# Kernel optimization log

Measured on AMD Instinct MI355X. Metric: run time of the kernel, lower is better.

Reference implementation:

```python
import jax, jax.numpy as jnp
import numpy as np

B, C, H, W = 32, 64, 64, 64
K = 512  # n_embeddings
D = 64   # embedding_dim


def setup_inputs() -> dict:
    key = jax.random.key(0)
    k1, k2 = jax.random.split(key)
    inputs = jax.random.normal(k1, (B, C, H, W), dtype=jnp.float32)
    embedding = jax.random.normal(k2, (K, D), dtype=jnp.float32)
    weight = jnp.ones((K,), dtype=jnp.float32)
    return {"inputs": inputs, "embedding": embedding, "weight": weight}


def reference(inputs, embedding, weight):
    # NCHW -> NHWC, flatten to [N, D]
    x = jnp.transpose(inputs, (0, 2, 3, 1))  # [B,H,W,D]
    input_shape = x.shape
    flat = x.reshape(-1, D)                  # [N,D], N = B*H*W
    n = flat.shape[0]

    usage = jnp.sum(weight >= 0.01)

    # squared Euclidean distances (argmin-equivalent to torch.cdist)
    d2 = (jnp.sum(flat * flat, axis=1, keepdims=True)
          - 2.0 * (flat @ embedding.T)
          + jnp.sum(embedding * embedding, axis=1))  # [N,K]
    indices = jnp.argmin(d2, axis=1)                 # [N]

    # one-hot assignment stats (scatter -> bincount form)
    counts = jnp.zeros((K,), dtype=flat.dtype).at[indices].add(1.0)
    avg_probs = counts / n
    perplexity = jnp.exp(-jnp.sum(avg_probs * jnp.log(avg_probs + 1e-10)))

    # straight-through quantization
    q = embedding[indices].reshape(input_shape)      # [B,H,W,D]
    quantized = jax.lax.stop_gradient(q) + x - jax.lax.stop_gradient(x)

    commitment_loss = jnp.mean((jax.lax.stop_gradient(quantized) - x) ** 2)

    quantized_nchw = jnp.transpose(quantized, (0, 3, 1, 2))
    return quantized_nchw, commitment_loss, perplexity, usage, indices
```

## Files before the change

kernel.cpp:

```cpp
#include <hip/hip_runtime.h>


typedef __attribute__((ext_vector_type(8))) _Float16 f16x8;
typedef __attribute__((ext_vector_type(4))) float f32x4;
typedef unsigned int uint;
typedef unsigned short ushort;

namespace {
constexpr int kC = 64, kH = 64, kW = 64;
constexpr int kK = 512, kD = 64;
constexpr int kHW = kH * kW;
constexpr int kCHW = kC * kHW;
constexpr int kN = 32 * kHW;
constexpr int kQElems = 32 * kC * kHW;
constexpr uint kGapFP = 21u;
}

__device__ __forceinline__ ushort hb(_Float16 h) { return __builtin_bit_cast(ushort, h); }
__device__ __forceinline__ uint umin(uint a, uint b) { return a < b ? a : b; }
__device__ __forceinline__ uint umax(uint a, uint b) { return a > b ? a : b; }

__device__ __forceinline__ void gld16(const void* g, void* l) {
  __builtin_amdgcn_global_load_lds(
      (const __attribute__((address_space(1))) uint*)g,
      (__attribute__((address_space(3))) uint*)l, 16, 0, 0);
}

__global__ __launch_bounds__(64) void vq_prep(const float* __restrict__ emb,
                                              ushort* __restrict__ embPh,
                                              ushort* __restrict__ embPl,
                                              float* __restrict__ enorm,
                                              uint* __restrict__ counts,
                                              uint* __restrict__ flag_count) {
  const int k = blockIdx.x * 64 + threadIdx.x;
  const float4* __restrict__ ep4 = (const float4*)(emb + k * kD);
  uint uh[32], ul[32];
  float s = 0.f;
#pragma unroll
  for (int j = 0; j < kD / 4; ++j) {
    const float4 v = ep4[j];
    s = fmaf(v.x, v.x, s); s = fmaf(v.y, v.y, s);
    s = fmaf(v.z, v.z, s); s = fmaf(v.w, v.w, s);
    const float e0 = v.x * 2048.f, e1 = v.y * 2048.f;
    const float e2 = v.z * 2048.f, e3 = v.w * 2048.f;
    const _Float16 h0 = (_Float16)e0, h1 = (_Float16)e1;
    const _Float16 h2 = (_Float16)e2, h3 = (_Float16)e3;
    const _Float16 l0 = (_Float16)(e0 - (float)h0);
    const _Float16 l1 = (_Float16)(e1 - (float)h1);
    const _Float16 l2 = (_Float16)(e2 - (float)h2);
    const _Float16 l3 = (_Float16)(e3 - (float)h3);
    uh[2 * j] = (uint)hb(h0) | ((uint)hb(h1) << 16);
    uh[2 * j + 1] = (uint)hb(h2) | ((uint)hb(h3) << 16);
    ul[2 * j] = (uint)hb(l0) | ((uint)hb(l1) << 16);
    ul[2 * j + 1] = (uint)hb(l2) | ((uint)hb(l3) << 16);
  }
  uint4* __restrict__ ph4 = (uint4*)embPh;
  uint4* __restrict__ pl4 = (uint4*)embPl;
#pragma unroll
  for (int cc = 0; cc < 8; ++cc) {
    const int dst = k * 8 + (cc ^ (k & 7));
    ph4[dst] = uint4{uh[4 * cc], uh[4 * cc + 1], uh[4 * cc + 2], uh[4 * cc + 3]};
    pl4[dst] = uint4{ul[4 * cc], ul[4 * cc + 1], ul[4 * cc + 2], ul[4 * cc + 3]};
  }
  enorm[k] = s;
  counts[k] = 0u;
  if (k == 0) *flag_count = 0u;
}

__global__ __launch_bounds__(512, 4) void vq_assign(
    const float* __restrict__ in, const float* __restrict__ emb,
    const ushort* __restrict__ embPh, const ushort* __restrict__ embPl,
    const float* __restrict__ enorm, float* __restrict__ idx_out,
    float* __restrict__ outq, uint* __restrict__ counts,
    float* __restrict__ partial, uint* __restrict__ flag_count,
    uint* __restrict__ flags, uint flag_cap) {
  __shared__ __align__(16) char lds[74240];
  char* __restrict__ xbh = lds;
  char* __restrict__ xbl = lds + 16384;
  char* __restrict__ ebh = lds + 32768;
  char* __restrict__ ebl = lds + 49152;
  uint* __restrict__ mm1 = (uint*)(lds + 65536);
  uint* __restrict__ mm2 = (uint*)(lds + 67584);
  float* __restrict__ xnp = (float*)(lds + 69632);
  uint* __restrict__ hist = (uint*)(lds + 71680);
  uint* __restrict__ fidx = (uint*)(lds + 73728);
  float* __restrict__ ldsE = (float*)lds;

  const int tid = threadIdx.x;
  const int lane = tid & 63;
  const int wv = __builtin_amdgcn_readfirstlane(tid >> 6);
  const int ph = wv >> 2;
  const int cs = wv & 3;
  const int c = lane & 15;
  const int g = lane >> 4;

  const int blk = blockIdx.x;
  const int bb = blk >> 5;
  const int hw0 = (blk & 31) << 7;
  const float* __restrict__ xp = in + (size_t)bb * kCHW + hw0 + ph * 64;

  hist[tid] = 0u;

  auto stageE = [&](int buf, int st) {
    const size_t src = (size_t)st * 8192 + cs * 2048;
    const int dst = buf * 8192 + cs * 2048;
#pragma unroll
    for (int i = 0; i < 2; ++i) {
      gld16((const char*)embPh + src + i * 1024 + lane * 16, ebh + dst + i * 1024);
      gld16((const char*)embPl + src + i * 1024 + lane * 16, ebl + dst + i * 1024);
    }
  };
  stageE(0, 0);

  float en_pre[8];
#pragma unroll
  for (int st = 0; st < 8; ++st)
    en_pre[st] = (enorm[st * 64 + cs * 16 + c] + 256.f) * 2048.f;

  {
    const int p = lane;
    uint uh[8], ul[8];
    float xn = 0.f;
#pragma unroll
    for (int j = 0; j < 8; ++j) {
      const float f0 = xp[(size_t)(cs * 16 + 2 * j) * kHW + p];
      const float f1 = xp[(size_t)(cs * 16 + 2 * j + 1) * kHW + p];
      xn = fmaf(f0, f0, xn);
      xn = fmaf(f1, f1, xn);
      const float m0 = -2.f * f0, m1f = -2.f * f1;
      const _Float16 h0 = (_Float16)m0, h1 = (_Float16)m1f;
      const _Float16 l0 = (_Float16)(m0 - (float)h0);
      const _Float16 l1 = (_Float16)(m1f - (float)h1);
      uh[j] = (uint)hb(h0) | ((uint)hb(h1) << 16);
      ul[j] = (uint)hb(l0) | ((uint)hb(l1) << 16);
    }
    const int row = ph * 64 + p;
    const int swz = (row & 7) << 4;
    const int o0 = (row * 128 + cs * 32) ^ swz;
    const int o1 = (row * 128 + cs * 32 + 16) ^ swz;
    *(uint4*)(xbh + o0) = uint4{uh[0], uh[1], uh[2], uh[3]};
    *(uint4*)(xbh + o1) = uint4{uh[4], uh[5], uh[6], uh[7]};
    *(uint4*)(xbl + o0) = uint4{ul[0], ul[1], ul[2], ul[3]};
    *(uint4*)(xbl + o1) = uint4{ul[4], ul[5], ul[6], ul[7]};
    xnp[cs * 128 + row] = xn;
  }
  __syncthreads();

  uint m1[16], m2[16];
#pragma unroll
  for (int i = 0; i < 16; ++i) { m1[i] = 0xFFFFFFFFu; m2[i] = 0xFFFFFFFFu; }

#pragma unroll
  for (int st = 0; st < 8; ++st) {
    if (st < 7) stageE((st & 1) ^ 1, st + 1);

    if (st < 7) {
      asm volatile("s_waitcnt vmcnt(4)" ::: "memory");
    } else {
      asm volatile("s_waitcnt vmcnt(0)" ::: "memory");
    }
    __builtin_amdgcn_sched_barrier(0);

    const int rowb = cs * 16 + c;
    const int swb = (rowb & 7) << 4;
    const int bbase = (st & 1) * 8192;
    const int ob0 = bbase + ((rowb * 128 + g * 16) ^ swb);
    const int ob1 = bbase + ((rowb * 128 + g * 16 + 64) ^ swb);
    const f16x8 bh0 = *(const f16x8*)(ebh + ob0);
    const f16x8 bh1 = *(const f16x8*)(ebh + ob1);
    const f16x8 bl0 = *(const f16x8*)(ebl + ob0);
    const f16x8 bl1 = *(const f16x8*)(ebl + ob1);
    const float en = en_pre[st];
    const uint kor = (uint)(st * 64 + cs * 16 + c);
    __builtin_amdgcn_s_setprio(1);
#pragma unroll
    for (int rt = 0; rt < 4; ++rt) {
      f16x8 ah[2], al[2];
#pragma unroll
      for (int s = 0; s < 2; ++s) {
        const int row = ph * 64 + rt * 16 + c;
        const int off = (row * 128 + g * 16 + s * 64) ^ ((row & 7) << 4);
        ah[s] = *(const f16x8*)(xbh + off);
        al[s] = *(const f16x8*)(xbl + off);
      }
      f32x4 acc0 = {en, en, en, en};
      f32x4 acc1 = {0.f, 0.f, 0.f, 0.f};
      acc0 = __builtin_amdgcn_mfma_f32_16x16x32_f16(ah[0], bh0, acc0, 0, 0, 0);
      acc1 = __builtin_amdgcn_mfma_f32_16x16x32_f16(ah[1], bh1, acc1, 0, 0, 0);
      acc0 = __builtin_amdgcn_mfma_f32_16x16x32_f16(ah[0], bl0, acc0, 0, 0, 0);
      acc1 = __builtin_amdgcn_mfma_f32_16x16x32_f16(ah[1], bl1, acc1, 0, 0, 0);
      acc0 = __builtin_amdgcn_mfma_f32_16x16x32_f16(al[0], bh0, acc0, 0, 0, 0);
      acc1 = __builtin_amdgcn_mfma_f32_16x16x32_f16(al[1], bh1, acc1, 0, 0, 0);
#pragma unroll
      for (int r = 0; r < 4; ++r) {
        const uint u = ((uint)(acc0[r] + acc1[r]) << 9) | kor;
        const int i = rt * 4 + r;
        const uint t = umax(m1[i], u);
        m1[i] = umin(m1[i], u);
        m2[i] = umin(m2[i], t);
      }
    }
    __builtin_amdgcn_s_setprio(0);

    asm volatile("s_waitcnt lgkmcnt(0)" ::: "memory");
    __builtin_amdgcn_sched_barrier(0);
    __builtin_amdgcn_s_barrier();
  }

#pragma unroll
  for (int i = 0; i < 16; ++i) {
    uint a1 = m1[i], a2 = m2[i];
#pragma unroll
    for (int off = 1; off < 16; off <<= 1) {
      const uint o1 = __shfl_xor(a1, off, 64);
      const uint o2 = __shfl_xor(a2, off, 64);
      const uint t = umax(a1, o1);
      a1 = umin(a1, o1);
      a2 = umin(umin(a2, o2), t);
    }
    m1[i] = a1; m2[i] = a2;
  }

  if (c == 0) {
#pragma unroll
    for (int i = 0; i < 16; ++i) {
      const int p = ph * 64 + (i >> 2) * 16 + g * 4 + (i & 3);
      mm1[cs * 128 + p] = m1[i];
      mm2[cs * 128 + p] = m2[i];
    }
  }
  __syncthreads();

  if (tid < 128) {
    uint a1 = mm1[tid], a2 = mm2[tid];
#pragma unroll
    for (int s = 1; s < 4; ++s) {
      const uint u1 = mm1[s * 128 + tid], u2 = mm2[s * 128 + tid];
      const uint t = umax(a1, u1);
      a1 = umin(a1, u1);
      a2 = umin(umin(a2, u2), t);
    }
    const uint bidx = a1 & 511u;
    fidx[tid] = bidx;
    idx_out[blk * 128 + tid] = (float)bidx;
    if (((a2 >> 9) - (a1 >> 9)) < kGapFP) {
      const uint slot = atomicAdd(flag_count, 1u);
      if (slot < flag_cap) flags[slot] = (uint)(blk * 128 + tid);
    }
    atomicAdd(&hist[bidx], 1u);

    const float xnorm = (xnp[tid] + xnp[128 + tid]) + (xnp[256 + tid] + xnp[384 + tid]);
    float d2 = fmaf((float)(a1 >> 9), 1.f / 2048.f, -256.f) + xnorm;
#pragma unroll
    for (int off = 32; off > 0; off >>= 1) d2 += __shfl_down(d2, off, 64);
    if ((tid & 63) == 0) partial[blk * 2 + (tid >> 6)] = d2;
  }
  __syncthreads();
  if (hist[tid]) atomicAdd(&counts[tid], hist[tid]);

#pragma unroll
  for (int pass = 0; pass < 4; ++pass) {
    const int r = pass * 32 + (tid >> 4);
    const int q = tid & 15;
    const float4 v = *(const float4*)(emb + fidx[r] * kD + q * 4);
    const int cswz = (q * 4) ^ (((r >> 4) & 7) << 3);
    *(float4*)(ldsE + r * 64 + cswz) = v;
  }
  __syncthreads();
  {
    const int ch = tid >> 3;
    const int wq = tid & 7;
    float* __restrict__ oq = outq + (size_t)bb * kCHW + (size_t)ch * kHW + hw0 + wq * 16;
    float4 vv[4];
#pragma unroll
    for (int i = 0; i < 16; ++i) {
      const int p = wq * 16 + i;
      const int cswz = ch ^ (((p >> 4) & 7) << 3);
      ((float*)vv)[i] = ldsE[p * 64 + cswz];
    }
#pragma unroll
    for (int i = 0; i < 4; ++i) *(float4*)(oq + i * 4) = vv[i];
  }
}

__global__ __launch_bounds__(256) void vq_refine_fin(
    const float* __restrict__ in, const float* __restrict__ emb,
    const float* __restrict__ weight, const uint* __restrict__ flag_count,
    const uint* __restrict__ flags, uint flag_cap, float* __restrict__ idx_out,
    float* __restrict__ outq, const uint* __restrict__ counts,
    const float* __restrict__ partial, float* __restrict__ out_scalars) {
  if (blockIdx.x == 256) {
    __shared__ float red[256];
    const int t = threadIdx.x;

    {
      const float a0 = (float)counts[t] / (float)kN;
      const float a1 = (float)counts[t + 256] / (float)kN;
      red[t] = a0 * logf(a0 + 1e-10f) + a1 * logf(a1 + 1e-10f);
    }
    __syncthreads();
#pragma unroll
    for (int off = 128; off > 0; off >>= 1) {
      if (t < off) red[t] += red[t + off];
      __syncthreads();
    }
    const float perp = expf(-red[0]);
    __syncthreads();

    {
      float a = 0.f;
#pragma unroll
      for (int j = 0; j < 8; ++j) a += partial[t + 256 * j];
      red[t] = a;
    }
    __syncthreads();
#pragma unroll
    for (int off = 128; off > 0; off >>= 1) {
      if (t < off) red[t] += red[t + off];
      __syncthreads();
    }
    const float loss = red[0] / (float)((long long)kN * (long long)kD);
    __syncthreads();

    red[t] = ((weight[t] >= 0.01f) ? 1.f : 0.f) +
             ((weight[t + 256] >= 0.01f) ? 1.f : 0.f);
    __syncthreads();
#pragma unroll
    for (int off = 128; off > 0; off >>= 1) {
      if (t < off) red[t] += red[t + off];
      __syncthreads();
    }
    if (t == 0) {
      out_scalars[0] = loss;
      out_scalars[1] = perp;
      out_scalars[2] = red[0];
    }
    return;
  }

  uint cnt = *flag_count;
  if (cnt > flag_cap) cnt = flag_cap;
  const int lane = threadIdx.x & 63;
  const uint wave_id = blockIdx.x * 4u + (threadIdx.x >> 6);
  const uint wave_stride = 256u * 4u;

  for (uint i = wave_id; i < cnt; i += wave_stride) {
    const int n = (int)flags[i];
    const int b = n >> 12;
    const int hw = n & 4095;
    const float* __restrict__ xp = in + (size_t)b * kCHW + hw;

    float xr[kD];
#pragma unroll
    for (int d = 0; d < kD; ++d) xr[d] = xp[(size_t)d * kHW];

    double best = 1e300;
    int bidx = 0;
#pragma unroll 1
    for (int kk = 0; kk < 8; ++kk) {
      const int k = lane * 8 + kk;
      const float4* __restrict__ ep4 = (const float4*)(emb + k * kD);
      double s0 = 0.0, s1 = 0.0;
#pragma unroll
      for (int j = 0; j < kD / 4; ++j) {
        const float4 e = ep4[j];
        const double d0 = (double)xr[4 * j + 0] - (double)e.x;
        const double d1 = (double)xr[4 * j + 1] - (double)e.y;
        const double d2 = (double)xr[4 * j + 2] - (double)e.z;
        const double d3 = (double)xr[4 * j + 3] - (double)e.w;
        s0 = fma(d0, d0, s0);
        s1 = fma(d1, d1, s1);
        s0 = fma(d2, d2, s0);
        s1 = fma(d3, d3, s1);
      }
      const double s = s0 + s1;
      if (s < best) { best = s; bidx = k; }
    }
#pragma unroll
    for (int off = 32; off > 0; off >>= 1) {
      const double ob = __shfl_xor(best, off, 64);
      const int oi = __shfl_xor(bidx, off, 64);
      if (ob < best || (ob == best && oi < bidx)) { best = ob; bidx = oi; }
    }
    if (lane == 0) idx_out[n] = (float)bidx;
    outq[(size_t)b * kCHW + (size_t)lane * kHW + hw] = emb[bidx * kD + lane];
  }
}

extern "C" void kernel_launch(void* const* d_in, const int* in_sizes, int n_in,
                              void* d_out, int out_size, void* d_ws, size_t ws_size,
                              hipStream_t stream) {
  const float* in = (const float*)d_in[0];
  const float* emb = (const float*)d_in[1];
  const float* weight = (const float*)d_in[2];
  float* out = (float*)d_out;

  float* ws_f = (float*)d_ws;
  uint* ws_u = (uint*)d_ws;
  ushort* embPh = (ushort*)d_ws;
  ushort* embPl = embPh + kK * kD;
  float* enorm = ws_f + 65536;
  uint* counts = ws_u + 66048;
  float* partial = ws_f + 66560;
  uint* flag_count = ws_u + 68608;
  uint* flags = ws_u + 68609;
  const size_t ws_elems = ws_size / 4;
  const uint flag_cap =
      (ws_elems > 68609)
          ? (uint)((ws_elems - 68609 < (size_t)kN) ? ws_elems - 68609 : (size_t)kN)
          : 0u;

  float* outq = out;
  float* out_scalars = out + kQElems;
  float* idx_out = out + kQElems + 3;

  vq_prep<<<8, 64, 0, stream>>>(emb, embPh, embPl, enorm, counts, flag_count);
  vq_assign<<<kN / 128, 512, 0, stream>>>(in, emb, embPh, embPl, enorm, idx_out,
                                          outq, counts, partial, flag_count, flags,
                                          flag_cap);
  vq_refine_fin<<<257, 256, 0, stream>>>(in, emb, weight, flag_count, flags,
                                         flag_cap, idx_out, outq, counts, partial,
                                         out_scalars);
}
```

Measured before the change: 84.10 us.

## Give each wave all codes for its own rows with private embedding staging

The assign kernel now uses 256 threads with 4 waves. Each wave owns 32 input rows and sweeps all 512 codes in 32 steps, double-buffering the embedding tiles in a private per-wave LDS region. This removes the cross-wave min/second-min merge through LDS and the per-stage block barriers, and shrinks LDS to 32 KB so more blocks fit on a CU. The costs are 4x more redundant embedding loads from global/L2, which each wave now fetches itself, plus a histogram done with direct global atomics and a larger partial-sum buffer.

```diff
diff --git a/kernel.cpp b/kernel.cpp
--- a/kernel.cpp
+++ b/kernel.cpp
@@ -67,64 +67,39 @@
   if (k == 0) *flag_count = 0u;
 }
 
-__global__ __launch_bounds__(512, 4) void vq_assign(
+__global__ __launch_bounds__(256, 5) void vq_assign(
     const float* __restrict__ in, const float* __restrict__ emb,
     const ushort* __restrict__ embPh, const ushort* __restrict__ embPl,
     const float* __restrict__ enorm, float* __restrict__ idx_out,
     float* __restrict__ outq, uint* __restrict__ counts,
     float* __restrict__ partial, uint* __restrict__ flag_count,
     uint* __restrict__ flags, uint flag_cap) {
-  __shared__ __align__(16) char lds[74240];
+  __shared__ __align__(16) char lds[32768];
   char* __restrict__ xbh = lds;
   char* __restrict__ xbl = lds + 16384;
-  char* __restrict__ ebh = lds + 32768;
-  char* __restrict__ ebl = lds + 49152;
-  uint* __restrict__ mm1 = (uint*)(lds + 65536);
-  uint* __restrict__ mm2 = (uint*)(lds + 67584);
-  float* __restrict__ xnp = (float*)(lds + 69632);
-  uint* __restrict__ hist = (uint*)(lds + 71680);
-  uint* __restrict__ fidx = (uint*)(lds + 73728);
-  float* __restrict__ ldsE = (float*)lds;
+  uint* __restrict__ fidx = (uint*)lds;
+  float* __restrict__ ldsE = (float*)(lds + 512);
 
   const int tid = threadIdx.x;
   const int lane = tid & 63;
   const int wv = __builtin_amdgcn_readfirstlane(tid >> 6);
-  const int ph = wv >> 2;
-  const int cs = wv & 3;
   const int c = lane & 15;
   const int g = lane >> 4;
 
   const int blk = blockIdx.x;
   const int bb = blk >> 5;
   const int hw0 = (blk & 31) << 7;
-  const float* __restrict__ xp = in + (size_t)bb * kCHW + hw0 + ph * 64;
-
-  hist[tid] = 0u;
-
-  auto stageE = [&](int buf, int st) {
-    const size_t src = (size_t)st * 8192 + cs * 2048;
-    const int dst = buf * 8192 + cs * 2048;
-#pragma unroll
-    for (int i = 0; i < 2; ++i) {
-      gld16((const char*)embPh + src + i * 1024 + lane * 16, ebh + dst + i * 1024);
-      gld16((const char*)embPl + src + i * 1024 + lane * 16, ebl + dst + i * 1024);
-    }
-  };
-  stageE(0, 0);
-
-  float en_pre[8];
-#pragma unroll
-  for (int st = 0; st < 8; ++st)
-    en_pre[st] = (enorm[st * 64 + cs * 16 + c] + 256.f) * 2048.f;
-
-  {
-    const int p = lane;
+  const float* __restrict__ xp = in + (size_t)bb * kCHW + hw0;
+
+  float xn = 0.f;
+#pragma unroll
+  for (int pp = 0; pp < 2; ++pp) {
+    const int p = pp * 64 + lane;
     uint uh[8], ul[8];
-    float xn = 0.f;
 #pragma unroll
     for (int j = 0; j < 8; ++j) {
-      const float f0 = xp[(size_t)(cs * 16 + 2 * j) * kHW + p];
-      const float f1 = xp[(size_t)(cs * 16 + 2 * j + 1) * kHW + p];
+      const float f0 = xp[(size_t)(wv * 16 + 2 * j) * kHW + p];
+      const float f1 = xp[(size_t)(wv * 16 + 2 * j + 1) * kHW + p];
       xn = fmaf(f0, f0, xn);
       xn = fmaf(f1, f1, xn);
       const float m0 = -2.f * f0, m1f = -2.f * f1;
@@ -134,63 +109,84 @@
       uh[j] = (uint)hb(h0) | ((uint)hb(h1) << 16);
       ul[j] = (uint)hb(l0) | ((uint)hb(l1) << 16);
     }
-    const int row = ph * 64 + p;
-    const int swz = (row & 7) << 4;
-    const int o0 = (row * 128 + cs * 32) ^ swz;
-    const int o1 = (row * 128 + cs * 32 + 16) ^ swz;
+    const int swz = (p & 7) << 4;
+    const int o0 = (p * 128 + wv * 32) ^ swz;
+    const int o1 = (p * 128 + wv * 32 + 16) ^ swz;
     *(uint4*)(xbh + o0) = uint4{uh[0], uh[1], uh[2], uh[3]};
     *(uint4*)(xbh + o1) = uint4{uh[4], uh[5], uh[6], uh[7]};
     *(uint4*)(xbl + o0) = uint4{ul[0], ul[1], ul[2], ul[3]};
     *(uint4*)(xbl + o1) = uint4{ul[4], ul[5], ul[6], ul[7]};
-    xnp[cs * 128 + row] = xn;
+  }
+  {
+    float xw = xn;
+#pragma unroll
+    for (int off = 32; off > 0; off >>= 1) xw += __shfl_down(xw, off, 64);
+    if (lane == 0) partial[blk * 8 + 4 + wv] = xw;
   }
   __syncthreads();
 
-  uint m1[16], m2[16];
-#pragma unroll
-  for (int i = 0; i < 16; ++i) { m1[i] = 0xFFFFFFFFu; m2[i] = 0xFFFFFFFFu; }
-
-#pragma unroll
-  for (int st = 0; st < 8; ++st) {
-    if (st < 7) stageE((st & 1) ^ 1, st + 1);
-
-    if (st < 7) {
+  f16x8 ah[2][2], al[2][2];
+#pragma unroll
+  for (int rt = 0; rt < 2; ++rt)
+#pragma unroll
+    for (int s = 0; s < 2; ++s) {
+      const int row = wv * 32 + rt * 16 + c;
+      const int off = (row * 128 + g * 16 + s * 64) ^ ((row & 7) << 4);
+      ah[rt][s] = *(const f16x8*)(xbh + off);
+      al[rt][s] = *(const f16x8*)(xbl + off);
+    }
+
+  float en_pre[32];
+#pragma unroll
+  for (int st = 0; st < 32; ++st)
+    en_pre[st] = (enorm[st * 16 + c] + 256.f) * 2048.f;
+  __syncthreads();
+
+  char* __restrict__ myE = lds + wv * 8192;
+  auto stageE = [&](int buf, int st) {
+    const size_t src = (size_t)st * 2048;
+    char* d = myE + buf * 4096;
+    gld16((const char*)embPh + src + lane * 16, d);
+    gld16((const char*)embPh + src + 1024 + lane * 16, d + 1024);
+    gld16((const char*)embPl + src + lane * 16, d + 2048);
+    gld16((const char*)embPl + src + 1024 + lane * 16, d + 3072);
+  };
+  stageE(0, 0);
+
+  uint m1[8], m2[8];
+#pragma unroll
+  for (int i = 0; i < 8; ++i) { m1[i] = 0xFFFFFFFFu; m2[i] = 0xFFFFFFFFu; }
+
+#pragma unroll
+  for (int st = 0; st < 32; ++st) {
+    if (st < 31) stageE((st & 1) ^ 1, st + 1);
+    if (st < 31) {
       asm volatile("s_waitcnt vmcnt(4)" ::: "memory");
     } else {
       asm volatile("s_waitcnt vmcnt(0)" ::: "memory");
     }
     __builtin_amdgcn_sched_barrier(0);
 
-    const int rowb = cs * 16 + c;
-    const int swb = (rowb & 7) << 4;
-    const int bbase = (st & 1) * 8192;
-    const int ob0 = bbase + ((rowb * 128 + g * 16) ^ swb);
-    const int ob1 = bbase + ((rowb * 128 + g * 16 + 64) ^ swb);
-    const f16x8 bh0 = *(const f16x8*)(ebh + ob0);
-    const f16x8 bh1 = *(const f16x8*)(ebh + ob1);
-    const f16x8 bl0 = *(const f16x8*)(ebl + ob0);
-    const f16x8 bl1 = *(const f16x8*)(ebl + ob1);
+    const char* bufp = myE + (st & 1) * 4096;
+    const int swb = (c & 7) << 4;
+    const int ob0 = (c * 128 + g * 16) ^ swb;
+    const int ob1 = (c * 128 + g * 16 + 64) ^ swb;
+    const f16x8 bh0 = *(const f16x8*)(bufp + ob0);
+    const f16x8 bh1 = *(const f16x8*)(bufp + ob1);
+    const f16x8 bl0 = *(const f16x8*)(bufp + 2048 + ob0);
+    const f16x8 bl1 = *(const f16x8*)(bufp + 2048 + ob1);
     const float en = en_pre[st];
-    const uint kor = (uint)(st * 64 + cs * 16 + c);
-    __builtin_amdgcn_s_setprio(1);
-#pragma unroll
-    for (int rt = 0; rt < 4; ++rt) {
-      f16x8 ah[2], al[2];
-#pragma unroll
-      for (int s = 0; s < 2; ++s) {
-        const int row = ph * 64 + rt * 16 + c;
-        const int off = (row * 128 + g * 16 + s * 64) ^ ((row & 7) << 4);
-        ah[s] = *(const f16x8*)(xbh + off);
-        al[s] = *(const f16x8*)(xbl + off);
-      }
+    const uint kor = (uint)(st * 16 + c);
+#pragma unroll
+    for (int rt = 0; rt < 2; ++rt) {
       f32x4 acc0 = {en, en, en, en};
       f32x4 acc1 = {0.f, 0.f, 0.f, 0.f};
-      acc0 = __builtin_amdgcn_mfma_f32_16x16x32_f16(ah[0], bh0, acc0, 0, 0, 0);
-      acc1 = __builtin_amdgcn_mfma_f32_16x16x32_f16(ah[1], bh1, acc1, 0, 0, 0);
-      acc0 = __builtin_amdgcn_mfma_f32_16x16x32_f16(ah[0], bl0, acc0, 0, 0, 0);
-      acc1 = __builtin_amdgcn_mfma_f32_16x16x32_f16(ah[1], bl1, acc1, 0, 0, 0);
-      acc0 = __builtin_amdgcn_mfma_f32_16x16x32_f16(al[0], bh0, acc0, 0, 0, 0);
-      acc1 = __builtin_amdgcn_mfma_f32_16x16x32_f16(al[1], bh1, acc1, 0, 0, 0);
+      acc0 = __builtin_amdgcn_mfma_f32_16x16x32_f16(ah[rt][0], bh0, acc0, 0, 0, 0);
+      acc1 = __builtin_amdgcn_mfma_f32_16x16x32_f16(ah[rt][1], bh1, acc1, 0, 0, 0);
+      acc0 = __builtin_amdgcn_mfma_f32_16x16x32_f16(ah[rt][0], bl0, acc0, 0, 0, 0);
+      acc1 = __builtin_amdgcn_mfma_f32_16x16x32_f16(ah[rt][1], bl1, acc1, 0, 0, 0);
+      acc0 = __builtin_amdgcn_mfma_f32_16x16x32_f16(al[rt][0], bh0, acc0, 0, 0, 0);
+      acc1 = __builtin_amdgcn_mfma_f32_16x16x32_f16(al[rt][1], bh1, acc1, 0, 0, 0);
 #pragma unroll
       for (int r = 0; r < 4; ++r) {
         const uint u = ((uint)(acc0[r] + acc1[r]) << 9) | kor;
@@ -200,15 +196,10 @@
         m2[i] = umin(m2[i], t);
       }
     }
-    __builtin_amdgcn_s_setprio(0);
-
-    asm volatile("s_waitcnt lgkmcnt(0)" ::: "memory");
-    __builtin_amdgcn_sched_barrier(0);
-    __builtin_amdgcn_s_barrier();
-  }
-
-#pragma unroll
-  for (int i = 0; i < 16; ++i) {
+  }
+
+#pragma unroll
+  for (int i = 0; i < 8; ++i) {
     uint a1 = m1[i], a2 = m2[i];
 #pragma unroll
     for (int off = 1; off < 16; off <<= 1) {
@@ -220,66 +211,58 @@
     }
     m1[i] = a1; m2[i] = a2;
   }
-
+  __syncthreads();
+
+  float d2 = 0.f;
   if (c == 0) {
 #pragma unroll
-    for (int i = 0; i < 16; ++i) {
-      const int p = ph * 64 + (i >> 2) * 16 + g * 4 + (i & 3);
-      mm1[cs * 128 + p] = m1[i];
-      mm2[cs * 128 + p] = m2[i];
-    }
-  }
+    for (int i = 0; i < 8; ++i) {
+      const int rt = i >> 2, r = i & 3;
+      const int p = wv * 32 + rt * 16 + g * 4 + r;
+      const int n = blk * 128 + p;
+      const uint bidx = m1[i] & 511u;
+      fidx[p] = bidx;
+      idx_out[n] = (float)bidx;
+      if (((m2[i] >> 9) - (m1[i] >> 9)) < kGapFP) {
+        const uint slot = atomicAdd(flag_count, 1u);
+        if (slot < flag_cap) flags[slot] = (uint)n;
+      }
+      atomicAdd(&counts[bidx], 1u);
+      d2 += fmaf((float)(m1[i] >> 9), 1.f / 2048.f, -256.f);
+    }
+  }
+#pragma unroll
+  for (int off = 32; off > 0; off >>= 1) d2 += __shfl_down(d2, off, 64);
+  if (lane == 0) partial[blk * 8 + wv] = d2;
   __syncthreads();
 
-  if (tid < 128) {
-    uint a1 = mm1[tid], a2 = mm2[tid];
-#pragma unroll
-    for (int s = 1; s < 4; ++s) {
-      const uint u1 = mm1[s * 128 + tid], u2 = mm2[s * 128 + tid];
-      const uint t = umax(a1, u1);
-      a1 = umin(a1, u1);
-      a2 = umin(umin(a2, u2), t);
-    }
-    const uint bidx = a1 & 511u;
-    fidx[tid] = bidx;
-    idx_out[blk * 128 + tid] = (float)bidx;
-    if (((a2 >> 9) - (a1 >> 9)) < kGapFP) {
-      const uint slot = atomicAdd(flag_count, 1u);
-      if (slot < flag_cap) flags[slot] = (uint)(blk * 128 + tid);
-    }
-    atomicAdd(&hist[bidx], 1u);
-
-    const float xnorm = (xnp[tid] + xnp[128 + tid]) + (xnp[256 + tid] + xnp[384 + tid]);
-    float d2 = fmaf((float)(a1 >> 9), 1.f / 2048.f, -256.f) + xnorm;
-#pragma unroll
-    for (int off = 32; off > 0; off >>= 1) d2 += __shfl_down(d2, off, 64);
-    if ((tid & 63) == 0) partial[blk * 2 + (tid >> 6)] = d2;
-  }
-  __syncthreads();
-  if (hist[tid]) atomicAdd(&counts[tid], hist[tid]);
-
-#pragma unroll
-  for (int pass = 0; pass < 4; ++pass) {
-    const int r = pass * 32 + (tid >> 4);
-    const int q = tid & 15;
-    const float4 v = *(const float4*)(emb + fidx[r] * kD + q * 4);
-    const int cswz = (q * 4) ^ (((r >> 4) & 7) << 3);
-    *(float4*)(ldsE + r * 64 + cswz) = v;
-  }
-  __syncthreads();
-  {
-    const int ch = tid >> 3;
-    const int wq = tid & 7;
-    float* __restrict__ oq = outq + (size_t)bb * kCHW + (size_t)ch * kHW + hw0 + wq * 16;
-    float4 vv[4];
-#pragma unroll
-    for (int i = 0; i < 16; ++i) {
-      const int p = wq * 16 + i;
-      const int cswz = ch ^ (((p >> 4) & 7) << 3);
-      ((float*)vv)[i] = ldsE[p * 64 + cswz];
-    }
-#pragma unroll
-    for (int i = 0; i < 4; ++i) *(float4*)(oq + i * 4) = vv[i];
+#pragma unroll
+  for (int pp = 0; pp < 2; ++pp) {
+#pragma unroll
+    for (int pass2 = 0; pass2 < 4; ++pass2) {
+      const int rr = pass2 * 16 + (tid >> 4);
+      const int q = tid & 15;
+      const float4 v = *(const float4*)(emb + fidx[pp * 64 + rr] * kD + q * 4);
+      const int cswz = (q * 4) ^ (((rr >> 4) & 3) << 3);
+      *(float4*)(ldsE + rr * 64 + cswz) = v;
+    }
+    __syncthreads();
+    {
+      const int ch = tid >> 2;
+      const int wq = tid & 3;
+      float* __restrict__ oq =
+          outq + (size_t)bb * kCHW + (size_t)ch * kHW + hw0 + pp * 64 + wq * 16;
+      float4 vv[4];
+#pragma unroll
+      for (int i = 0; i < 16; ++i) {
+        const int p = wq * 16 + i;
+        const int cswz = ch ^ (((p >> 4) & 3) << 3);
+        ((float*)vv)[i] = ldsE[p * 64 + cswz];
+      }
+#pragma unroll
+      for (int i = 0; i < 4; ++i) *(float4*)(oq + i * 4) = vv[i];
+    }
+    __syncthreads();
   }
 }
 
@@ -310,7 +293,7 @@
     {
       float a = 0.f;
 #pragma unroll
-      for (int j = 0; j < 8; ++j) a += partial[t + 256 * j];
+      for (int j = 0; j < 32; ++j) a += partial[t + 256 * j];
       red[t] = a;
     }
     __syncthreads();
@@ -402,12 +385,12 @@
   float* enorm = ws_f + 65536;
   uint* counts = ws_u + 66048;
   float* partial = ws_f + 66560;
-  uint* flag_count = ws_u + 68608;
-  uint* flags = ws_u + 68609;
+  uint* flag_count = ws_u + 74752;
+  uint* flags = ws_u + 74753;
   const size_t ws_elems = ws_size / 4;
   const uint flag_cap =
-      (ws_elems > 68609)
-          ? (uint)((ws_elems - 68609 < (size_t)kN) ? ws_elems - 68609 : (size_t)kN)
+      (ws_elems > 74753)
+          ? (uint)((ws_elems - 74753 < (size_t)kN) ? ws_elems - 74753 : (size_t)kN)
           : 0u;
 
   float* outq = out;
@@ -415,7 +398,7 @@
   float* idx_out = out + kQElems + 3;
 
   vq_prep<<<8, 64, 0, stream>>>(emb, embPh, embPl, enorm, counts, flag_count);
-  vq_assign<<<kN / 128, 512, 0, stream>>>(in, emb, embPh, embPl, enorm, idx_out,
+  vq_assign<<<kN / 128, 256, 0, stream>>>(in, emb, embPh, embPl, enorm, idx_out,
                                           outq, counts, partial, flag_count, flags,
                                           flag_cap);
   vq_refine_fin<<<257, 256, 0, stream>>>(in, emb, weight, flag_count, flags,
```

Measured after the change: 211.9 us. 2.52x slower.
